# Performance work log

Measured on AMD Instinct MI355X. Metric: run time of the kernel, lower is better.

## Reference

```python
import jax, jax.numpy as jnp
import numpy as np

KSIZE = 15
SIGMA = 3.0
PAD = KSIZE // 2


def _gauss_kernel2d():
    g = jnp.arange(KSIZE, dtype=jnp.float32) - KSIZE // 2
    g = jnp.exp(-(g ** 2) / (2.0 * SIGMA * SIGMA))
    g = g / g.sum()
    return g[:, None] * g[None, :]  # [15,15]


def _depthwise_blur(x, k2):
    # x: [B,C,H,W]; 15x15 Gaussian applied per channel (matches per-channel F.conv2d loop)
    C = x.shape[1]
    kernel = jnp.broadcast_to(k2[None, None], (C, 1, KSIZE, KSIZE))
    return jax.lax.conv_general_dilated(
        x, kernel, window_strides=(1, 1), padding=[(PAD, PAD), (PAD, PAD)],
        feature_group_count=C, dimension_numbers=("NCHW", "OIHW", "NCHW"))


def setup_inputs() -> dict:
    key = jax.random.key(0)
    B, C, H, W = 4, 3, 1024, 1024
    x = jax.random.uniform(key, (B, C, H, W), dtype=jnp.float32)
    f32 = lambda v: jnp.asarray(v, dtype=jnp.float32)
    return {
        "x": x,
        "gains": jnp.array([1.1, 1.0, 0.9], dtype=jnp.float32),
        "gamma": f32(0.9),
        "shadow_boost": f32(0.1),
        "highlight_reduce": f32(0.1),
        "brightness": f32(0.05),
        "contrast": f32(1.1),
        "enhance_amount": f32(0.8),
        "softness": f32(0.6),
        "intensity": f32(0.3),
        "rotation": f32(30.0),
        "hardness": f32(2.0),
    }


def reference(x, gains, gamma, shadow_boost, highlight_reduce, brightness,
              contrast, enhance_amount, softness, intensity, rotation, hardness):
    B, C, H, W = x.shape
    k2 = _gauss_kernel2d()

    # WhiteBalanceAdjustment
    x = x * gains.reshape(1, C, 1, 1)
    # ToneCurveAdjustment
    x = jnp.power(x, gamma)
    # ShadowHighlightEnhancement
    hi = jax.nn.sigmoid((x - 0.5) * 10.0)
    x = jnp.clip(x + shadow_boost * (1.0 - hi) - highlight_reduce * hi, 0.0, 1.0)
    # GlobalBrightnessContrastAdjustment
    x = jnp.clip(contrast * (x - 0.5) + 0.5 + brightness, 0.0, 1.0)
    # LocalContrastEnhancement
    local_mean = _depthwise_blur(x, k2)
    x = x + enhance_amount * (x - local_mean)
    # SoftnessFilter
    blurred = _depthwise_blur(x, k2)
    x = softness * blurred + (1.0 - softness) * x
    # GradientNDAdjustment
    ys = jnp.linspace(-1.0, 1.0, H, dtype=jnp.float32)
    xs = jnp.linspace(-1.0, 1.0, W, dtype=jnp.float32)
    grid_y, grid_x = jnp.meshgrid(ys, xs, indexing="ij")
    theta = rotation * (np.pi / 180.0)
    grid_rot = grid_x * jnp.cos(theta) + grid_y * jnp.sin(theta)
    mask = jax.nn.sigmoid(-hardness * grid_rot)[None, None]  # [1,1,H,W]
    x = jnp.clip(x * (1.0 - intensity * mask), 0.0, 1.0)

    return jnp.clip(x, 0.0, 1.0)
```

## Files before the change

kernel.cpp:

```cpp
#include <hip/hip_runtime.h>
#include <math.h>

#define HH 1024
#define WW 1024
#define NPLANES 12
#define PLANE (HH * WW)
#define NTOT (NPLANES * PLANE)

#define TW 64
#define TH 64
#define RH 92
#define RB 78
#define PH 80
#define LDSF (156 * PH)

struct W15 { float w[15]; };

__device__ inline float chain1(float t, float gain, float gamma, float sb,
                               float hr, float br, float ct) {
    t = t * gain;
    t = __builtin_amdgcn_exp2f(gamma * __log2f(t));
    float hi = __fdividef(1.0f, 1.0f + __expf((0.5f - t) * 10.0f));
    t = t + sb * (1.0f - hi) - hr * hi;
    t = fminf(fmaxf(t, 0.0f), 1.0f);
    t = ct * (t - 0.5f) + 0.5f + br;
    return fminf(fmaxf(t, 0.0f), 1.0f);
}

__device__ inline int b1r(int r) { return (r < 64) ? (92 + r) : (r + 14); }
__device__ inline int swq(int pr, int q) { return pr * PH + ((q ^ (pr & 3)) << 2); }
__device__ inline int sws(int pr, int j) {
    return pr * PH + ((((j >> 2) ^ (pr & 3)) << 2) | (j & 3));
}

__device__ inline void dot16(const float* f, const W15& wk, float* o) {
#pragma unroll
    for (int j = 0; j < 16; ++j) {
        float a = 0.0f, b = 0.0f;
#pragma unroll
        for (int k = 0; k < 8; ++k)  a += wk.w[k] * f[j + 1 + k];
#pragma unroll
        for (int k = 8; k < 15; ++k) b += wk.w[k] * f[j + 1 + k];
        o[j] = a + b;
    }
}

__device__ inline float dot15(const float* win, const W15& wk) {
    float a = 0.0f, b = 0.0f;
#pragma unroll
    for (int k = 0; k < 8; ++k)  a += wk.w[k] * win[k];
#pragma unroll
    for (int k = 8; k < 15; ++k) b += wk.w[k] * win[k];
    return a + b;
}

__device__ inline void tile_map(int& p, int& x0, int& y0, bool& edge) {
    int L = (blockIdx.z * gridDim.y + blockIdx.y) * gridDim.x + blockIdx.x;
    int xcd = L & 7;
    int t   = L >> 3;
    int g   = xcd * 384 + t;
    p = g >> 8;
    int w  = g & 255;
    int ty = w >> 4, tx = w & 15;
    x0 = tx * TW; y0 = ty * TH;
    edge = (tx == 0) || (tx == 15) || (ty == 0) || (ty == 15);
}

__global__ __launch_bounds__(256) void k_point(
    const float4* __restrict__ x, float4* __restrict__ o,
    const float* __restrict__ gains,
    const float* __restrict__ pg, const float* __restrict__ psb,
    const float* __restrict__ phr, const float* __restrict__ pbr,
    const float* __restrict__ pct)
{
    int i = blockIdx.x * blockDim.x + threadIdx.x;
    if (i >= NTOT / 4) return;
    int c = ((i * 4) / PLANE) % 3;
    float gain = gains[c];
    float gamma = *pg, sb = *psb, hr = *phr, br = *pbr, ct = *pct;

    float4 v = x[i];
    float* pv = (float*)&v;
#pragma unroll
    for (int j = 0; j < 4; ++j)
        pv[j] = chain1(pv[j], gain, gamma, sb, hr, br, ct);
    o[i] = v;
}

__global__ __launch_bounds__(256, 3) void k_fused(
    const float* __restrict__ x1, float* __restrict__ dst,
    const float* __restrict__ penh,
    const float* __restrict__ psoft, const float* __restrict__ pint,
    const float* __restrict__ prot, const float* __restrict__ phard,
    W15 wk)
{
    __shared__ float lds[LDSF];

    int p, x0, y0; bool edge;
    tile_map(p, x0, y0, edge);
    const int tid = threadIdx.x;
    const int tx  = tid & 63;
    const int ty  = tid >> 6;

    const float* __restrict__ plane = x1 + (size_t)p * PLANE;

#pragma unroll
    for (int it = 0; it < 2; ++it) {
        int u = tid + 256 * it;
        if (u < RH * 5) {
            int r = u / 5, s = u - 5 * r;
            int gy  = y0 - 14 + r;
            int gxa = x0 + 16 * s - 16;
            float f[32];
            if (!edge) {
                const float* rp = plane + (size_t)gy * WW + gxa;
#pragma unroll
                for (int i = 0; i < 8; ++i)
                    *(float4*)&f[4 * i] = *(const float4*)(rp + 4 * i);
            } else {
                bool rowin = (unsigned)gy < HH;
                const float* rp = plane + (size_t)(rowin ? gy : 0) * WW;
#pragma unroll
                for (int e2 = 0; e2 < 32; ++e2) {
                    int gx2 = gxa + e2;
                    f[e2] = (rowin && (unsigned)gx2 < WW) ? rp[gx2] : 0.0f;
                }
            }
            float o[16];
            dot16(f, wk, o);
#pragma unroll
            for (int qq = 0; qq < 4; ++qq)
                *(float4*)&lds[swq(r, 4 * s + qq)] = *(float4*)&o[4 * qq];
        }
    }

    float cc[16];
    {
        const float* pc0 = plane + (size_t)(y0 + ty * 16) * WW + (x0 + tx);
#pragma unroll
        for (int jj = 0; jj < 16; ++jj) cc[jj] = pc0[(size_t)jj * WW];
    }
    __syncthreads();

    if (tid < 240) {
        int j = tid % 80, band = tid / 80;
        int rb0 = band * 28;
        int nj  = (band == 2) ? 22 : 28;
        bool xin = (unsigned)(x0 - 8 + j) < WW;
        float win[15];
#pragma unroll
        for (int k = 0; k < 14; ++k) win[k] = lds[sws(rb0 + k, j)];
#pragma unroll
        for (int jj = 0; jj < 28; ++jj) {
            if (jj < nj) {
                int rl = rb0 + jj;
                win[14] = lds[sws(rl + 14, j)];
                float v = dot15(win, wk);
                if (edge) {
                    int gy = y0 - 7 + rl;
                    if (!((unsigned)gy < HH) || !xin) v = 0.0f;
                }
                lds[sws(b1r(rl), j)] = v;
#pragma unroll
                for (int k = 0; k < 14; ++k) win[k] = win[k + 1];
            }
        }
    }
    __syncthreads();

#pragma unroll
    for (int it = 0; it < 2; ++it) {
        int u = tid + 256 * it;
        if (u < RB * 4) {
            int rb = u >> 2, s = u & 3;
            int pb = b1r(rb);
            float f[32];
#pragma unroll
            for (int i = 0; i < 8; ++i)
                *(float4*)&f[4 * i] = *(const float4*)&lds[swq(pb, 4 * s + i)];
            float o[16];
            dot16(f, wk, o);
#pragma unroll
            for (int qq = 0; qq < 4; ++qq)
                *(float4*)&lds[swq(rb, 4 * s + qq)] = *(float4*)&o[4 * qq];
        }
    }
    __syncthreads();

    const float e     = *penh;
    const float sf    = *psoft;
    const float inten = *pint;
    const float hard  = *phard;
    const float theta = (*prot) * 0.017453292519943295f;
    const float cth = __cosf(theta), sth = __sinf(theta);
    const int   gx    = x0 + tx;
    const float gbase = (-1.0f + 2.0f * (float)gx * (1.0f / (float)(WW - 1))) * cth;
    const float ce    = 1.0f + e;

    float bb[16];
#pragma unroll
    for (int jj = 0; jj < 16; ++jj)
        bb[jj] = lds[sws(b1r(ty * 16 + jj + 7), tx + 8)];

    float win[15];
#pragma unroll
    for (int k = 0; k < 14; ++k) win[k] = lds[sws(ty * 16 + k, tx)];

    float* __restrict__ dstP = dst + (size_t)p * PLANE;
#pragma unroll
    for (int jj = 0; jj < 16; ++jj) {
        win[14] = lds[sws(ty * 16 + jj + 14, tx)];
        float B2  = dot15(win, wk);
        float x2c = ce * cc[jj] - e * bb[jj];
        float bx2 = ce * bb[jj] - e * B2;
        float v   = sf * bx2 + (1.0f - sf) * x2c;
        int   y   = y0 + ty * 16 + jj;
        float gyn = -1.0f + 2.0f * (float)y * (1.0f / (float)(HH - 1));
        float mask = __fdividef(1.0f, 1.0f + __expf(hard * (gbase + gyn * sth)));
        v = v * (1.0f - inten * mask);
        v = fminf(fmaxf(v, 0.0f), 1.0f);
        dstP[(size_t)y * WW + gx] = v;
#pragma unroll
        for (int k = 0; k < 14; ++k) win[k] = win[k + 1];
    }
}

extern "C" void kernel_launch(void* const* d_in, const int* in_sizes, int n_in,
                              void* d_out, int out_size, void* d_ws, size_t ws_size,
                              hipStream_t stream)
{
    const float* x       = (const float*)d_in[0];
    const float* gains   = (const float*)d_in[1];
    const float* p_gamma = (const float*)d_in[2];
    const float* p_sb    = (const float*)d_in[3];
    const float* p_hr    = (const float*)d_in[4];
    const float* p_br    = (const float*)d_in[5];
    const float* p_ct    = (const float*)d_in[6];
    const float* p_enh   = (const float*)d_in[7];
    const float* p_soft  = (const float*)d_in[8];
    const float* p_int   = (const float*)d_in[9];
    const float* p_rot   = (const float*)d_in[10];
    const float* p_hard  = (const float*)d_in[11];

    float* X1 = (float*)d_ws;

    W15 wk;
    {
        double g[15], sum = 0.0;
        for (int i = 0; i < 15; ++i) { double d = (double)(i - 7); g[i] = exp(-d * d / 18.0); sum += g[i]; }
        for (int i = 0; i < 15; ++i) wk.w[i] = (float)(g[i] / sum);
    }

    k_point<<<dim3(NTOT / 4 / 256), dim3(256), 0, stream>>>(
        (const float4*)x, (float4*)X1, gains, p_gamma, p_sb, p_hr, p_br, p_ct);

    dim3 grid(WW / TW, HH / TH, NPLANES);
    k_fused<<<grid, dim3(256), 0, stream>>>(
        X1, (float*)d_out, p_enh, p_soft, p_int, p_rot, p_hard, wk);
}
```

Measured before the change: 184.2 us.

## Fuse pointwise tone chain into blur kernel, dropping intermediate buffer

The separate pointwise kernel that applied white balance, gamma, shadow/highlight and contrast is removed. That chain is now computed inside the fused blur kernel on each loaded halo element and center pixel. This removes a full-size write and re-read of the intermediate plane and one kernel launch. In exchange, the transcendental-heavy chain is recomputed for overlapping halo pixels (about 30/16 times in the horizontal pass, plus the center reload), which raises ALU work and register pressure.

```diff
diff --git a/kernel.cpp b/kernel.cpp
--- a/kernel.cpp
+++ b/kernel.cpp
@@ -5,7 +5,6 @@
 #define WW 1024
 #define NPLANES 12
 #define PLANE (HH * WW)
-#define NTOT (NPLANES * PLANE)
 
 #define TW 64
 #define TH 64
@@ -66,30 +65,12 @@
     edge = (tx == 0) || (tx == 15) || (ty == 0) || (ty == 15);
 }
 
-__global__ __launch_bounds__(256) void k_point(
-    const float4* __restrict__ x, float4* __restrict__ o,
+__global__ __launch_bounds__(256, 3) void k_fused(
+    const float* __restrict__ x, float* __restrict__ dst,
     const float* __restrict__ gains,
     const float* __restrict__ pg, const float* __restrict__ psb,
     const float* __restrict__ phr, const float* __restrict__ pbr,
-    const float* __restrict__ pct)
-{
-    int i = blockIdx.x * blockDim.x + threadIdx.x;
-    if (i >= NTOT / 4) return;
-    int c = ((i * 4) / PLANE) % 3;
-    float gain = gains[c];
-    float gamma = *pg, sb = *psb, hr = *phr, br = *pbr, ct = *pct;
-
-    float4 v = x[i];
-    float* pv = (float*)&v;
-#pragma unroll
-    for (int j = 0; j < 4; ++j)
-        pv[j] = chain1(pv[j], gain, gamma, sb, hr, br, ct);
-    o[i] = v;
-}
-
-__global__ __launch_bounds__(256, 3) void k_fused(
-    const float* __restrict__ x1, float* __restrict__ dst,
-    const float* __restrict__ penh,
+    const float* __restrict__ pct, const float* __restrict__ penh,
     const float* __restrict__ psoft, const float* __restrict__ pint,
     const float* __restrict__ prot, const float* __restrict__ phard,
     W15 wk)
@@ -102,7 +83,9 @@
     const int tx  = tid & 63;
     const int ty  = tid >> 6;
 
-    const float* __restrict__ plane = x1 + (size_t)p * PLANE;
+    const float* __restrict__ plane = x + (size_t)p * PLANE;
+    const float gain  = gains[p % 3];
+    const float gamma = *pg, sb = *psb, hr = *phr, br = *pbr, ct = *pct;
 
 #pragma unroll
     for (int it = 0; it < 2; ++it) {
@@ -111,23 +94,39 @@
             int r = u / 5, s = u - 5 * r;
             int gy  = y0 - 14 + r;
             int gxa = x0 + 16 * s - 16;
-            float f[32];
+            float o[16];
+            bool rowin = (unsigned)gy < HH;
             if (!edge) {
                 const float* rp = plane + (size_t)gy * WW + gxa;
+                float f[32];
 #pragma unroll
                 for (int i = 0; i < 8; ++i)
                     *(float4*)&f[4 * i] = *(const float4*)(rp + 4 * i);
+#pragma unroll
+                for (int e2 = 1; e2 < 31; ++e2)
+                    f[e2] = chain1(f[e2], gain, gamma, sb, hr, br, ct);
+                dot16(f, wk, o);
+            } else if (rowin) {
+                const float* rp = plane + (size_t)gy * WW;
+                float f[32];
+#pragma unroll
+                for (int i = 0; i < 8; ++i) {
+                    int gq = gxa + 4 * i;
+                    float4 v = make_float4(0.f, 0.f, 0.f, 0.f);
+                    if (gq >= 0 && gq + 3 < WW) {
+                        v = *(const float4*)(rp + gq);
+                        float* pv = (float*)&v;
+#pragma unroll
+                        for (int q2 = 0; q2 < 4; ++q2)
+                            pv[q2] = chain1(pv[q2], gain, gamma, sb, hr, br, ct);
+                    }
+                    *(float4*)&f[4 * i] = v;
+                }
+                dot16(f, wk, o);
             } else {
-                bool rowin = (unsigned)gy < HH;
-                const float* rp = plane + (size_t)(rowin ? gy : 0) * WW;
-#pragma unroll
-                for (int e2 = 0; e2 < 32; ++e2) {
-                    int gx2 = gxa + e2;
-                    f[e2] = (rowin && (unsigned)gx2 < WW) ? rp[gx2] : 0.0f;
-                }
+#pragma unroll
+                for (int j = 0; j < 16; ++j) o[j] = 0.0f;
             }
-            float o[16];
-            dot16(f, wk, o);
 #pragma unroll
             for (int qq = 0; qq < 4; ++qq)
                 *(float4*)&lds[swq(r, 4 * s + qq)] = *(float4*)&o[4 * qq];
@@ -139,6 +138,9 @@
         const float* pc0 = plane + (size_t)(y0 + ty * 16) * WW + (x0 + tx);
 #pragma unroll
         for (int jj = 0; jj < 16; ++jj) cc[jj] = pc0[(size_t)jj * WW];
+#pragma unroll
+        for (int jj = 0; jj < 16; ++jj)
+            cc[jj] = chain1(cc[jj], gain, gamma, sb, hr, br, ct);
     }
     __syncthreads();
 
@@ -242,8 +244,6 @@
     const float* p_rot   = (const float*)d_in[10];
     const float* p_hard  = (const float*)d_in[11];
 
-    float* X1 = (float*)d_ws;
-
     W15 wk;
     {
         double g[15], sum = 0.0;
@@ -251,10 +251,8 @@
         for (int i = 0; i < 15; ++i) wk.w[i] = (float)(g[i] / sum);
     }
 
-    k_point<<<dim3(NTOT / 4 / 256), dim3(256), 0, stream>>>(
-        (const float4*)x, (float4*)X1, gains, p_gamma, p_sb, p_hr, p_br, p_ct);
-
     dim3 grid(WW / TW, HH / TH, NPLANES);
     k_fused<<<grid, dim3(256), 0, stream>>>(
-        X1, (float*)d_out, p_enh, p_soft, p_int, p_rot, p_hard, wk);
-}
+        x, (float*)d_out, gains, p_gamma, p_sb, p_hr, p_br, p_ct,
+        p_enh, p_soft, p_int, p_rot, p_hard, wk);
+}
```

Measured after the change: 201.2 us. 1.09x slower.
